# Performance work log

Measured on AMD Instinct MI355X. Metric: run time of the kernel, lower is better.

Reference implementation:

```python
import jax, jax.numpy as jnp
import numpy as np
import math

NUM_HEADS = 12
POS_BND = 16                 # patch_num
RPE_NUM = 2 * POS_BND + 1    # 33
LOGIT_SCALE_MAX = math.log(1.0 / 0.01)
EPS_NORM = 1e-12


def setup_inputs() -> dict:
    key = jax.random.key(0)
    ks = jax.random.split(key, 8)
    L, N, C = 257, 32, 768   # L = 16*16 patches + 1 CLS
    H, W = 16, 16
    x = jax.random.normal(ks[0], (L, N, C), dtype=jnp.float32)
    depth = jax.random.uniform(ks[1], (N, 1, H, W), dtype=jnp.float32)
    in_proj_w = jax.random.normal(ks[2], (3 * C, C), dtype=jnp.float32) * 0.02
    in_proj_b = jnp.zeros((3 * C,), dtype=jnp.float32)
    out_proj_w = jax.random.normal(ks[3], (C, C), dtype=jnp.float32) * 0.02
    out_proj_b = jnp.zeros((C,), dtype=jnp.float32)
    rpe_table = jax.random.normal(ks[4], (3 * RPE_NUM, NUM_HEADS), dtype=jnp.float32) * 0.02
    logit_scale = jnp.log(10.0) * jnp.ones((NUM_HEADS, 1, 1), dtype=jnp.float32)
    return {
        "x": x, "depth": depth,
        "in_proj_w": in_proj_w, "in_proj_b": in_proj_b,
        "out_proj_w": out_proj_w, "out_proj_b": out_proj_b,
        "rpe_table": rpe_table, "logit_scale": logit_scale,
    }


def _rpe_bias(depth, rpe_table):
    # depth: (B, 1, H, W) -> bias (B*num_heads, H*W, H*W)
    d = depth[:, 0]                              # (B, H, W)
    B, H, W = d.shape
    ii, jj = jnp.meshgrid(jnp.arange(H), jnp.arange(W), indexing="ij")
    xg = (jj.astype(jnp.float32) / (W - 1))[None].repeat(B, axis=0)   # (B,H,W)
    yg = (ii.astype(jnp.float32) / (H - 1))[None].repeat(B, axis=0)
    z_min = d.min(axis=(-2, -1), keepdims=True)
    z_max = d.max(axis=(-2, -1), keepdims=True)
    z = (d - z_min) / (z_max - z_min + 1e-8)
    coords = jnp.stack([xg, yg, z], axis=-1).reshape(B, H * W, 3)     # (B,HW,3)
    rel = coords[:, :, None, :] - coords[:, None, :, :]               # (B,HW,HW,3)
    idx = jnp.clip(jnp.round(rel * POS_BND).astype(jnp.int32), -POS_BND, POS_BND)
    idx = idx + POS_BND + jnp.arange(3, dtype=jnp.int32) * RPE_NUM    # (B,HW,HW,3)
    bias = rpe_table[idx].sum(axis=3)                                 # (B,HW,HW,heads)
    bias = bias.transpose(0, 3, 1, 2)                                 # (B,heads,HW,HW)
    return bias.reshape(-1, H * W, H * W)


def reference(x, depth, in_proj_w, in_proj_b, out_proj_w, out_proj_b, rpe_table, logit_scale):
    L, N, C = x.shape
    Hn = NUM_HEADS
    hd = C // Hn
    qkv = x @ in_proj_w.T + in_proj_b                     # (L,N,3C)
    q, k, v = jnp.split(qkv, 3, axis=-1)
    def to_heads(t):
        return t.reshape(L, N * Hn, hd).transpose(1, 0, 2)  # (N*Hn, L, hd)
    q, k, v = to_heads(q), to_heads(k), to_heads(v)
    # scaled-cosine attention: normalized q,k then clamped exp(log-scale)
    qn = q / jnp.maximum(jnp.linalg.norm(q, axis=-1, keepdims=True), EPS_NORM)
    kn = k / jnp.maximum(jnp.linalg.norm(k, axis=-1, keepdims=True), EPS_NORM)
    attn = jnp.einsum("bld,bmd->blm", qn, kn)             # (N*Hn, L, L)
    scale = jnp.exp(jnp.minimum(logit_scale, LOGIT_SCALE_MAX))   # (Hn,1,1)
    attn = (attn.reshape(N, Hn, L, L) * scale).reshape(N * Hn, L, L)
    # relative-position bias on patch tokens (skip CLS at index 0)
    res = _rpe_bias(depth, rpe_table)                     # (N*Hn, L-1, L-1)
    attn = attn.at[:, 1:, 1:].add(res)
    attn = jax.nn.softmax(attn, axis=-1)
    out = jnp.einsum("blm,bmd->bld", attn, v)             # (N*Hn, L, hd)
    out = out.transpose(1, 0, 2).reshape(L, N, C)
    out = out @ out_proj_w.T + out_proj_b
    return out, attn
```

## Files before the change

kernel.cpp:

```cpp
#include <hip/hip_runtime.h>
#include <math.h>

#define L_TOK 257
#define N_B 32
#define C_DIM 768
#define N_H 12
#define HD 64
#define BH (N_B * N_H)
#define M_TOK (L_TOK * N_B)
#define HW 256
#define RPE_NUM 33
#define LOGIT_MAX 4.6051701859880913680f
#define VT_STRIDE 264

typedef unsigned short ushort;
typedef unsigned int uint;
typedef __attribute__((ext_vector_type(8))) short short8;
typedef __attribute__((ext_vector_type(4))) float f32x4;

__device__ __forceinline__ ushort f2bf_rn(float f) {
  uint u = __float_as_uint(f);
  uint r = (u + 0x7FFF + ((u >> 16) & 1)) >> 16;
  return (ushort)r;
}
__device__ __forceinline__ float bf2f(ushort h) {
  return __uint_as_float(((uint)h) << 16);
}

__global__ __launch_bounds__(256)
void cvt_split(const float* __restrict__ src, ushort* __restrict__ hi,
               ushort* __restrict__ lo, int n) {
  int i = (blockIdx.x * 256 + threadIdx.x) * 4;
  if (i + 3 >= n + 3) return;
  if (i + 3 < n) {
    float4 v = *(const float4*)(src + i);
    ushort h0 = f2bf_rn(v.x), h1 = f2bf_rn(v.y), h2 = f2bf_rn(v.z), h3 = f2bf_rn(v.w);
    ushort l0 = f2bf_rn(v.x - bf2f(h0)), l1 = f2bf_rn(v.y - bf2f(h1));
    ushort l2 = f2bf_rn(v.z - bf2f(h2)), l3 = f2bf_rn(v.w - bf2f(h3));
    *(ushort4*)(hi + i) = make_ushort4(h0, h1, h2, h3);
    *(ushort4*)(lo + i) = make_ushort4(l0, l1, l2, l3);
  } else {
    for (int k = i; k < n; ++k) {
      float vv = src[k];
      ushort h = f2bf_rn(vv);
      hi[k] = h; lo[k] = f2bf_rn(vv - bf2f(h));
    }
  }
}

__global__ __launch_bounds__(256)
void gemm_mfma_split(const ushort* __restrict__ Ahi, const ushort* __restrict__ Alo,
                     const ushort* __restrict__ Bhi, const ushort* __restrict__ Blo,
                     const float* __restrict__ bias, float* __restrict__ Cout,
                     int M, int Nn, int K) {
  __shared__ __align__(16) ushort lds[4 * 128 * 32];
  ushort* sAh = lds;
  ushort* sAl = lds + 4096;
  ushort* sBh = lds + 8192;
  ushort* sBl = lds + 12288;

  const int t = threadIdx.x;
  const int wave = t >> 6, lane = t & 63;
  const int wm = (wave & 1) * 64;
  const int wn = (wave >> 1) * 64;
  const int m0 = blockIdx.x * 128;
  const int n0 = blockIdx.y * 128;

  const int ar = t >> 2;
  const int ac = (t & 3) * 8;
  const uint ldsOff = (uint)(t & 192) * 16;

  const int frm = lane & 15;
  const int frk = (lane >> 4) * 8;

  f32x4 acc[4][4] = {};

  for (int k0 = 0; k0 < K; k0 += 32) {
#pragma unroll
    for (int half = 0; half < 2; ++half) {
      int rA = m0 + half * 64 + ar; if (rA > M - 1) rA = M - 1;
      int rB = n0 + half * 64 + ar;
      size_t gA = (size_t)rA * K + k0 + ac;
      size_t gB = (size_t)rB * K + k0 + ac;
      uint so = (uint)half * 4096 + ldsOff;
      __builtin_amdgcn_global_load_lds(
          (const __attribute__((address_space(1))) void*)(Ahi + gA),
          (__attribute__((address_space(3))) void*)((char*)sAh + so), 16, 0, 0);
      __builtin_amdgcn_global_load_lds(
          (const __attribute__((address_space(1))) void*)(Alo + gA),
          (__attribute__((address_space(3))) void*)((char*)sAl + so), 16, 0, 0);
      __builtin_amdgcn_global_load_lds(
          (const __attribute__((address_space(1))) void*)(Bhi + gB),
          (__attribute__((address_space(3))) void*)((char*)sBh + so), 16, 0, 0);
      __builtin_amdgcn_global_load_lds(
          (const __attribute__((address_space(1))) void*)(Blo + gB),
          (__attribute__((address_space(3))) void*)((char*)sBl + so), 16, 0, 0);
    }
    __syncthreads();

    short8 ah[4], al[4], bh[4], bl[4];
#pragma unroll
    for (int i = 0; i < 4; ++i) {
      int r = wm + i * 16 + frm;
      ah[i] = *(const short8*)(sAh + r * 32 + frk);
      al[i] = *(const short8*)(sAl + r * 32 + frk);
      int c = wn + i * 16 + frm;
      bh[i] = *(const short8*)(sBh + c * 32 + frk);
      bl[i] = *(const short8*)(sBl + c * 32 + frk);
    }
#pragma unroll
    for (int i = 0; i < 4; ++i)
#pragma unroll
      for (int j = 0; j < 4; ++j) {
        acc[i][j] = __builtin_amdgcn_mfma_f32_16x16x32_bf16(ah[i], bh[j], acc[i][j], 0, 0, 0);
        acc[i][j] = __builtin_amdgcn_mfma_f32_16x16x32_bf16(ah[i], bl[j], acc[i][j], 0, 0, 0);
        acc[i][j] = __builtin_amdgcn_mfma_f32_16x16x32_bf16(al[i], bh[j], acc[i][j], 0, 0, 0);
      }
    __syncthreads();
  }

  const int ecol = lane & 15;
#pragma unroll
  for (int j = 0; j < 4; ++j) {
    int col = n0 + wn + j * 16 + ecol;
    float bv = bias[col];
#pragma unroll
    for (int i = 0; i < 4; ++i) {
      int rbase = m0 + wm + i * 16 + (lane >> 4) * 4;
#pragma unroll
      for (int r = 0; r < 4; ++r) {
        int row = rbase + r;
        if (row < M) Cout[(size_t)row * Nn + col] = acc[i][j][r] + bv;
      }
    }
  }
}

__global__ __launch_bounds__(256)
void repack_norm(const float* __restrict__ qkv,
                 ushort* __restrict__ qhi, ushort* __restrict__ qlo,
                 ushort* __restrict__ khi, ushort* __restrict__ klo,
                 float* __restrict__ v) {
  int gw = blockIdx.x * 4 + (threadIdx.x >> 6);
  int lane = threadIdx.x & 63;
  int b = gw / L_TOK, l = gw - b * L_TOK;
  int n = b / N_H, h = b - n * N_H;
  size_t base = (size_t)(l * N_B + n) * (3 * C_DIM) + h * HD + lane;
  float q = qkv[base];
  float k = qkv[base + C_DIM];
  float vv = qkv[base + 2 * C_DIM];
  float sq = q * q, sk = k * k;
#pragma unroll
  for (int o = 32; o > 0; o >>= 1) {
    sq += __shfl_down(sq, o);
    sk += __shfl_down(sk, o);
  }
  sq = __shfl(sq, 0);
  sk = __shfl(sk, 0);
  float iq = 1.0f / fmaxf(sqrtf(sq), 1e-12f);
  float ik = 1.0f / fmaxf(sqrtf(sk), 1e-12f);
  float qn_ = q * iq, kn_ = k * ik;
  size_t ob = (size_t)(b * L_TOK + l) * HD + lane;
  ushort qh = f2bf_rn(qn_);
  qhi[ob] = qh; qlo[ob] = f2bf_rn(qn_ - bf2f(qh));
  ushort kh = f2bf_rn(kn_);
  khi[ob] = kh; klo[ob] = f2bf_rn(kn_ - bf2f(kh));
  v[ob] = vv;
}

__global__ __launch_bounds__(256)
void vt_make(const float* __restrict__ v, ushort* __restrict__ vthi,
             ushort* __restrict__ vtlo) {
  __shared__ float sT[64][65];
  const int b = blockIdx.x;
  const int t = threadIdx.x;
  const float* vb = v + (size_t)b * L_TOK * HD;
  ushort* vh = vthi + (size_t)b * HD * VT_STRIDE;
  ushort* vl = vtlo + (size_t)b * HD * VT_STRIDE;
  for (int k0 = 0; k0 < 256; k0 += 64) {
#pragma unroll
    for (int p = 0; p < 16; ++p) {
      int idx = p * 256 + t;
      int k = idx >> 6, d = idx & 63;
      sT[d][k] = vb[(size_t)(k0 + k) * HD + d];
    }
    __syncthreads();
#pragma unroll
    for (int p = 0; p < 16; ++p) {
      int idx = p * 256 + t;
      int d = idx >> 6, k = idx & 63;
      float val = sT[d][k];
      ushort h = f2bf_rn(val);
      vh[(size_t)d * VT_STRIDE + k0 + k] = h;
      vl[(size_t)d * VT_STRIDE + k0 + k] = f2bf_rn(val - bf2f(h));
    }
    __syncthreads();
  }
  if (t < HD) {
    float val = vb[(size_t)256 * HD + t];
    ushort h = f2bf_rn(val);
    vh[(size_t)t * VT_STRIDE + 256] = h;
    vl[(size_t)t * VT_STRIDE + 256] = f2bf_rn(val - bf2f(h));
  }
}

__global__ __launch_bounds__(256)
void attn_mfma(const ushort* __restrict__ qhi, const ushort* __restrict__ qlo,
               const ushort* __restrict__ khi, const ushort* __restrict__ klo,
               const float* __restrict__ depth, const float* __restrict__ rpe,
               const float* __restrict__ lscale, float* __restrict__ P) {
  __shared__ __align__(16) ushort sKh[256 * 72];
  __shared__ __align__(16) ushort sKl[256 * 72];
  __shared__ float cz_s[HW];
  __shared__ float txd[32], tyd[32], tzt[36];
  __shared__ float red_s[16];
  __shared__ float s256[4][16];

  const int tile = blockIdx.x;
  const int b = blockIdx.y;
  const int n = b / N_H, h = b - n * N_H;
  const int t = threadIdx.x;
  const int lane = t & 63, wave = t >> 6;

  float dval = depth[n * HW + t];
  float mn = dval, mx = dval;
#pragma unroll
  for (int o = 32; o > 0; o >>= 1) {
    mn = fminf(mn, __shfl_down(mn, o));
    mx = fmaxf(mx, __shfl_down(mx, o));
  }
  if (lane == 0) { red_s[wave] = mn; red_s[8 + wave] = mx; }
  __syncthreads();
  float zmin = fminf(fminf(red_s[0], red_s[1]), fminf(red_s[2], red_s[3]));
  float zmax = fmaxf(fmaxf(red_s[8], red_s[9]), fmaxf(red_s[10], red_s[11]));
  float den = zmax - zmin + 1e-8f;
  cz_s[t] = (dval - zmin) / den;
  if (t < 31) {
    int d = t - 15;
    int ix = (int)rintf((float)d * (16.0f / 15.0f));
    ix = max(-16, min(16, ix));
    txd[t] = rpe[(ix + 16) * N_H + h];
    tyd[t] = rpe[(RPE_NUM + ix + 16) * N_H + h];
  }
  if (t < RPE_NUM) tzt[t] = rpe[(2 * RPE_NUM + t) * N_H + h];
  const float scale = expf(fminf(lscale[h], LOGIT_MAX));

  const ushort* khb = khi + (size_t)b * L_TOK * HD;
  const ushort* klb = klo + (size_t)b * L_TOK * HD;
#pragma unroll
  for (int it = 0; it < 8; ++it) {
    int idx = it * 256 + t;
    int j = idx >> 3, c = (idx & 7) * 8;
    *(uint4*)(sKh + j * 72 + c) = *(const uint4*)(khb + (size_t)j * HD + c);
    *(uint4*)(sKl + j * 72 + c) = *(const uint4*)(klb + (size_t)j * HD + c);
  }
  __syncthreads();

  const int qrow = tile * 64 + 16 * wave;
  const size_t qoff = ((size_t)b * L_TOK + qrow + (lane & 15)) * HD + (lane >> 4) * 8;
  short8 qh0 = *(const short8*)(qhi + qoff);
  short8 qh1 = *(const short8*)(qhi + qoff + 32);
  short8 ql0 = *(const short8*)(qlo + qoff);
  short8 ql1 = *(const short8*)(qlo + qoff + 32);

  f32x4 acc[16] = {};
#pragma unroll
  for (int jt = 0; jt < 16; ++jt) {
    const ushort* bp = sKh + (jt * 16 + (lane & 15)) * 72 + (lane >> 4) * 8;
    const ushort* bq = sKl + (jt * 16 + (lane & 15)) * 72 + (lane >> 4) * 8;
    short8 bh0 = *(const short8*)(bp);
    short8 bh1 = *(const short8*)(bp + 32);
    short8 bl0 = *(const short8*)(bq);
    short8 bl1 = *(const short8*)(bq + 32);
    acc[jt] = __builtin_amdgcn_mfma_f32_16x16x32_bf16(qh0, bh0, acc[jt], 0, 0, 0);
    acc[jt] = __builtin_amdgcn_mfma_f32_16x16x32_bf16(qh1, bh1, acc[jt], 0, 0, 0);
    acc[jt] = __builtin_amdgcn_mfma_f32_16x16x32_bf16(qh0, bl0, acc[jt], 0, 0, 0);
    acc[jt] = __builtin_amdgcn_mfma_f32_16x16x32_bf16(qh1, bl1, acc[jt], 0, 0, 0);
    acc[jt] = __builtin_amdgcn_mfma_f32_16x16x32_bf16(ql0, bh0, acc[jt], 0, 0, 0);
    acc[jt] = __builtin_amdgcn_mfma_f32_16x16x32_bf16(ql1, bh1, acc[jt], 0, 0, 0);
  }

  {
    const ushort* k6h = khb + (size_t)256 * HD + (lane >> 4) * 8;
    const ushort* k6l = klb + (size_t)256 * HD + (lane >> 4) * 8;
    float p = 0.f;
#pragma unroll
    for (int j = 0; j < 8; ++j) {
      float kf0 = bf2f(k6h[j]) + bf2f(k6l[j]);
      float kf1 = bf2f(k6h[32 + j]) + bf2f(k6l[32 + j]);
      float qf0 = bf2f((ushort)qh0[j]) + bf2f((ushort)ql0[j]);
      float qf1 = bf2f((ushort)qh1[j]) + bf2f((ushort)ql1[j]);
      p = fmaf(qf0, kf0, fmaf(qf1, kf1, p));
    }
    p += __shfl_xor(p, 16);
    p += __shfl_xor(p, 32);
    if (lane < 16) s256[wave][lane] = p;
  }

  const int g = lane >> 4, c0 = lane & 15;

  float lg6[4];
#pragma unroll
  for (int r = 0; r < 4; ++r) {
    int gi = tile * 64 + 16 * wave + 4 * g + r;
    float d6 = s256[wave][4 * g + r];
    float bz = 0.f;
    if (gi >= 1) {
      int dx = ((gi - 1) & 15) - 15;
      int dy = ((gi - 1) >> 4) - 15;
      float rz = (cz_s[gi - 1] - cz_s[255]) * 16.0f;
      int iz = (int)rintf(rz); iz = max(-16, min(16, iz));
      bz = txd[dx + 15] + tyd[dy + 15] + tzt[iz + 16];
    }
    lg6[r] = scale * d6 + bz;
  }

#pragma unroll
  for (int jt = 0; jt < 16; ++jt) {
    int col = jt * 16 + c0;
#pragma unroll
    for (int r = 0; r < 4; ++r) {
      int gi = tile * 64 + 16 * wave + 4 * g + r;
      float lv = scale * acc[jt][r];
      if (col >= 1 && gi >= 1) {
        int dx = ((gi - 1) & 15) - ((col - 1) & 15);
        int dy = ((gi - 1) >> 4) - ((col - 1) >> 4);
        float rz = (cz_s[gi - 1] - cz_s[col - 1]) * 16.0f;
        int iz = (int)rintf(rz); iz = max(-16, min(16, iz));
        lv += txd[dx + 15] + tyd[dy + 15] + tzt[iz + 16];
      }
      acc[jt][r] = lv;
    }
  }

  float* Pb_ = P + (size_t)b * L_TOK * L_TOK;
#pragma unroll
  for (int r = 0; r < 4; ++r) {
    int gi = tile * 64 + 16 * wave + 4 * g + r;
    float m = acc[0][r];
#pragma unroll
    for (int jt = 1; jt < 16; ++jt) m = fmaxf(m, acc[jt][r]);
#pragma unroll
    for (int o = 1; o < 16; o <<= 1) m = fmaxf(m, __shfl_xor(m, o));
    m = fmaxf(m, lg6[r]);
    float s = 0.f;
#pragma unroll
    for (int jt = 0; jt < 16; ++jt) {
      float e = __expf(acc[jt][r] - m);
      acc[jt][r] = e;
      s += e;
    }
#pragma unroll
    for (int o = 1; o < 16; o <<= 1) s += __shfl_xor(s, o);
    float e6 = __expf(lg6[r] - m);
    float inv = 1.0f / (s + e6);
    float* Prow = Pb_ + (size_t)gi * L_TOK;
#pragma unroll
    for (int jt = 0; jt < 16; ++jt)
      Prow[jt * 16 + c0] = acc[jt][r] * inv;
    if (c0 == 0) Prow[256] = e6 * inv;
  }
}

__global__ __launch_bounds__(256)
void attn_row256(const ushort* __restrict__ qhi, const ushort* __restrict__ qlo,
                 const ushort* __restrict__ khi, const ushort* __restrict__ klo,
                 const float* __restrict__ depth, const float* __restrict__ rpe,
                 const float* __restrict__ lscale, float* __restrict__ P) {
  __shared__ float qs[HD];
  __shared__ float cz_s[HW];
  __shared__ float txd[32], tyd[32], tzt[36];
  __shared__ float red_s[16];
  __shared__ float lg6_sh;

  const int b = blockIdx.x;
  const int n = b / N_H, h = b - n * N_H;
  const int t = threadIdx.x;
  const int lane = t & 63, wave = t >> 6;

  float dval = depth[n * HW + t];
  float mn = dval, mx = dval;
#pragma unroll
  for (int o = 32; o > 0; o >>= 1) {
    mn = fminf(mn, __shfl_down(mn, o));
    mx = fmaxf(mx, __shfl_down(mx, o));
  }
  if (lane == 0) { red_s[wave] = mn; red_s[8 + wave] = mx; }
  __syncthreads();
  float zmin = fminf(fminf(red_s[0], red_s[1]), fminf(red_s[2], red_s[3]));
  float zmax = fmaxf(fmaxf(red_s[8], red_s[9]), fmaxf(red_s[10], red_s[11]));
  float den = zmax - zmin + 1e-8f;
  cz_s[t] = (dval - zmin) / den;
  if (t < 31) {
    int d = t - 15;
    int ix = (int)rintf((float)d * (16.0f / 15.0f));
    ix = max(-16, min(16, ix));
    txd[t] = rpe[(ix + 16) * N_H + h];
    tyd[t] = rpe[(RPE_NUM + ix + 16) * N_H + h];
  }
  if (t < RPE_NUM) tzt[t] = rpe[(2 * RPE_NUM + t) * N_H + h];
  const float scale = expf(fminf(lscale[h], LOGIT_MAX));

  const size_t q6 = ((size_t)b * L_TOK + 256) * HD;
  if (t < HD) qs[t] = bf2f(qhi[q6 + t]) + bf2f(qlo[q6 + t]);
  __syncthreads();

  const ushort* krh = khi + ((size_t)b * L_TOK + t) * HD;
  const ushort* krl = klo + ((size_t)b * L_TOK + t) * HD;
  float dot = 0.f;
#pragma unroll
  for (int c = 0; c < HD; c += 8) {
    ushort4 hv0 = *(const ushort4*)(krh + c);
    ushort4 hv1 = *(const ushort4*)(krh + c + 4);
    ushort4 lv0 = *(const ushort4*)(krl + c);
    ushort4 lv1 = *(const ushort4*)(krl + c + 4);
    dot = fmaf(bf2f(hv0.x) + bf2f(lv0.x), qs[c + 0], dot);
    dot = fmaf(bf2f(hv0.y) + bf2f(lv0.y), qs[c + 1], dot);
    dot = fmaf(bf2f(hv0.z) + bf2f(lv0.z), qs[c + 2], dot);
    dot = fmaf(bf2f(hv0.w) + bf2f(lv0.w), qs[c + 3], dot);
    dot = fmaf(bf2f(hv1.x) + bf2f(lv1.x), qs[c + 4], dot);
    dot = fmaf(bf2f(hv1.y) + bf2f(lv1.y), qs[c + 5], dot);
    dot = fmaf(bf2f(hv1.z) + bf2f(lv1.z), qs[c + 6], dot);
    dot = fmaf(bf2f(hv1.w) + bf2f(lv1.w), qs[c + 7], dot);
  }

  float lg;
  {
    float bsum = 0.f;
    if (t >= 1) {
      int dx = 15 - ((t - 1) & 15);
      int dy = 15 - ((t - 1) >> 4);
      float rz = (cz_s[255] - cz_s[t - 1]) * 16.0f;
      int iz = (int)rintf(rz); iz = max(-16, min(16, iz));
      bsum = txd[dx + 15] + tyd[dy + 15] + tzt[iz + 16];
    }
    lg = scale * dot + bsum;
  }

  if (wave == 0) {
    const ushort* k6h = khi + q6;
    const ushort* k6l = klo + q6;
    float pp = (bf2f(k6h[lane]) + bf2f(k6l[lane])) * qs[lane];
#pragma unroll
    for (int o = 32; o > 0; o >>= 1) pp += __shfl_down(pp, o);
    if (lane == 0) {
      float bz = txd[15] + tyd[15] + tzt[16];
      lg6_sh = scale * pp + bz;
    }
  }

  float m = lg;
#pragma unroll
  for (int o = 32; o > 0; o >>= 1) m = fmaxf(m, __shfl_down(m, o));
  if (lane == 0) red_s[wave] = m;
  __syncthreads();
  float M = fmaxf(fmaxf(red_s[0], red_s[1]), fmaxf(red_s[2], red_s[3]));
  M = fmaxf(M, lg6_sh);
  float e = __expf(lg - M);
  float s = e;
#pragma unroll
  for (int o = 32; o > 0; o >>= 1) s += __shfl_down(s, o);
  if (lane == 0) red_s[8 + wave] = s;
  __syncthreads();
  float e6 = __expf(lg6_sh - M);
  float S = (red_s[8] + red_s[9]) + (red_s[10] + red_s[11]) + e6;
  float inv = 1.0f / S;
  float* Prow = P + (size_t)b * L_TOK * L_TOK + (size_t)256 * L_TOK;
  Prow[t] = e * inv;
  if (t == 0) Prow[256] = e6 * inv;
}

__global__ __launch_bounds__(256)
void pv_mfma(const float* __restrict__ P, const ushort* __restrict__ vthi,
             const ushort* __restrict__ vtlo, const float* __restrict__ v,
             float* __restrict__ out_lnc) {
  const int b = blockIdx.y;
  const int n = b / N_H, h = b - n * N_H;
  const int t = threadIdx.x;
  const int lane = t & 63, wave = t >> 6;
  const int rbase = blockIdx.x * 128 + wave * 32;
  const float* Pb = P + (size_t)b * L_TOK * L_TOK;
  const ushort* vh = vthi + (size_t)b * HD * VT_STRIDE;
  const ushort* vl = vtlo + (size_t)b * HD * VT_STRIDE;

  const int fm = lane & 15, fk = (lane >> 4) * 8;
  f32x4 acc[2][4] = {};

  for (int k0 = 0; k0 < 256; k0 += 32) {
    short8 ah[2], al[2], bh[4], bl[4];
#pragma unroll
    for (int i = 0; i < 2; ++i) {
      const float* pr = Pb + (size_t)(rbase + i * 16 + fm) * L_TOK + k0 + fk;
#pragma unroll
      for (int j = 0; j < 8; ++j) {
        float pv_ = pr[j];
        ushort hh = f2bf_rn(pv_);
        ah[i][j] = (short)hh;
        al[i][j] = (short)f2bf_rn(pv_ - bf2f(hh));
      }
    }
#pragma unroll
    for (int j = 0; j < 4; ++j) {
      const ushort* bp = vh + (size_t)(j * 16 + fm) * VT_STRIDE + k0 + fk;
      const ushort* bq = vl + (size_t)(j * 16 + fm) * VT_STRIDE + k0 + fk;
      bh[j] = *(const short8*)bp;
      bl[j] = *(const short8*)bq;
    }
#pragma unroll
    for (int i = 0; i < 2; ++i)
#pragma unroll
      for (int j = 0; j < 4; ++j) {
        acc[i][j] = __builtin_amdgcn_mfma_f32_16x16x32_bf16(ah[i], bh[j], acc[i][j], 0, 0, 0);
        acc[i][j] = __builtin_amdgcn_mfma_f32_16x16x32_bf16(ah[i], bl[j], acc[i][j], 0, 0, 0);
        acc[i][j] = __builtin_amdgcn_mfma_f32_16x16x32_bf16(al[i], bh[j], acc[i][j], 0, 0, 0);
        acc[i][j] = __builtin_amdgcn_mfma_f32_16x16x32_bf16(al[i], bl[j], acc[i][j], 0, 0, 0);
      }
  }

  const int g = lane >> 4;
  float v6[4];
#pragma unroll
  for (int j = 0; j < 4; ++j)
    v6[j] = v[((size_t)b * L_TOK + 256) * HD + j * 16 + fm];
#pragma unroll
  for (int i = 0; i < 2; ++i)
#pragma unroll
    for (int r = 0; r < 4; ++r) {
      int row = rbase + i * 16 + g * 4 + r;
      float p6 = Pb[(size_t)row * L_TOK + 256];
#pragma unroll
      for (int j = 0; j < 4; ++j) acc[i][j][r] += p6 * v6[j];
    }

#pragma unroll
  for (int i = 0; i < 2; ++i)
#pragma unroll
    for (int r = 0; r < 4; ++r) {
      int row = rbase + i * 16 + g * 4 + r;
      size_t o = ((size_t)row * N_B + n) * C_DIM + h * HD;
#pragma unroll
      for (int j = 0; j < 4; ++j)
        out_lnc[o + j * 16 + fm] = acc[i][j][r];
    }

  if (blockIdx.x == 0 && t < HD) {
    const float* Prow = Pb + (size_t)256 * L_TOK;
    const float* vb = v + (size_t)b * L_TOK * HD;
    float sum = 0.f;
    for (int k = 0; k < L_TOK; ++k)
      sum = fmaf(Prow[k], vb[(size_t)k * HD + t], sum);
    out_lnc[((size_t)256 * N_B + n) * C_DIM + h * HD + t] = sum;
  }
}

extern "C" void kernel_launch(void* const* d_in, const int* in_sizes, int n_in,
                              void* d_out, int out_size, void* d_ws, size_t ws_size,
                              hipStream_t stream) {
  const float* x      = (const float*)d_in[0];
  const float* depth  = (const float*)d_in[1];
  const float* w_in   = (const float*)d_in[2];
  const float* b_in   = (const float*)d_in[3];
  const float* w_out  = (const float*)d_in[4];
  const float* b_out  = (const float*)d_in[5];
  const float* rpe    = (const float*)d_in[6];
  const float* lscale = (const float*)d_in[7];
  float* out = (float*)d_out;
  float* ws = (float*)d_ws;

  float* qkv      = ws;
  float* attn_lnc = ws;
  float* v        = ws + 18948096;
  ushort* qhi = (ushort*)(ws + 25264128);
  ushort* qlo = qhi + 6316032;
  ushort* khi = qlo + 6316032;
  ushort* klo = khi + 6316032;
  ushort* wihi = (ushort*)(ws + 37896192);
  ushort* wilo = wihi + 1769472;
  ushort* wohi = wilo + 1769472;
  ushort* wolo = wohi + 589824;
  ushort* xhi = qhi;
  ushort* xlo = qlo;
  ushort* ahi = (ushort*)(qkv + 6316032);
  ushort* alo = ahi + 6316032;
  ushort* vthi = (ushort*)(ws + 6316032);
  ushort* vtlo = vthi + 6488064;
  float* Pout = out + 6316032;

  cvt_split<<<6168, 256, 0, stream>>>(x, xhi, xlo, 6316032);
  cvt_split<<<1728, 256, 0, stream>>>(w_in, wihi, wilo, 1769472);
  cvt_split<<<576, 256, 0, stream>>>(w_out, wohi, wolo, 589824);

  gemm_mfma_split<<<dim3(65, 18), 256, 0, stream>>>(xhi, xlo, wihi, wilo, b_in, qkv,
                                                    M_TOK, 3 * C_DIM, C_DIM);
  repack_norm<<<24672, 256, 0, stream>>>(qkv, qhi, qlo, khi, klo, v);
  vt_make<<<BH, 256, 0, stream>>>(v, vthi, vtlo);
  attn_mfma<<<dim3(4, BH), 256, 0, stream>>>(qhi, qlo, khi, klo, depth, rpe, lscale, Pout);
  attn_row256<<<BH, 256, 0, stream>>>(qhi, qlo, khi, klo, depth, rpe, lscale, Pout);
  pv_mfma<<<dim3(2, BH), 256, 0, stream>>>(Pout, vthi, vtlo, v, attn_lnc);

  cvt_split<<<6168, 256, 0, stream>>>(attn_lnc, ahi, alo, 6316032);
  gemm_mfma_split<<<dim3(65, 6), 256, 0, stream>>>(ahi, alo, wohi, wolo, b_out, out,
                                                   M_TOK, C_DIM, C_DIM);
}
```

Measured before the change: 522.7 us.

## Fuse QKV GEMM epilogue with head repack/normalization and fuse PV output split

The QKV GEMM epilogue now does the per-head L2 normalization, the bf16 hi/lo split and the scatter into head-major q/k/v buffers. This removes the separate repack_norm pass and the fp32 qkv intermediate. The PV kernel writes the bf16 hi/lo split of its output directly, which drops the cvt_split pass before the output projection. Both GEMMs switch to 1D grids with an XCD-aware block swizzle for better L2 locality; the epilogue's scattered stores may be less coalesced.

```diff
diff --git a/kernel.cpp b/kernel.cpp
--- a/kernel.cpp
+++ b/kernel.cpp
@@ -12,6 +12,8 @@
 #define RPE_NUM 33
 #define LOGIT_MAX 4.6051701859880913680f
 #define VT_STRIDE 264
+#define MT_Q 65
+#define NT_Q 18
 
 typedef unsigned short ushort;
 typedef unsigned int uint;
@@ -25,6 +27,13 @@
 }
 __device__ __forceinline__ float bf2f(ushort h) {
   return __uint_as_float(((uint)h) << 16);
+}
+
+__device__ __forceinline__ int xcd_swz(int wid, int nwg) {
+  int q = nwg >> 3, r = nwg & 7;
+  int xcd = wid & 7, pos = wid >> 3;
+  int base = (xcd < r) ? xcd * (q + 1) : r * (q + 1) + (xcd - r) * q;
+  return base + pos;
 }
 
 __global__ __launch_bounds__(256)
@@ -63,8 +72,10 @@
   const int wave = t >> 6, lane = t & 63;
   const int wm = (wave & 1) * 64;
   const int wn = (wave >> 1) * 64;
-  const int m0 = blockIdx.x * 128;
-  const int n0 = blockIdx.y * 128;
+  const int mt = (M + 127) >> 7;
+  const int wid = xcd_swz(blockIdx.x, gridDim.x);
+  const int m0 = (wid % mt) * 128;
+  const int n0 = (wid / mt) * 128;
 
   const int ar = t >> 2;
   const int ac = (t & 3) * 8;
@@ -137,35 +148,126 @@
 }
 
 __global__ __launch_bounds__(256)
-void repack_norm(const float* __restrict__ qkv,
-                 ushort* __restrict__ qhi, ushort* __restrict__ qlo,
-                 ushort* __restrict__ khi, ushort* __restrict__ klo,
-                 float* __restrict__ v) {
-  int gw = blockIdx.x * 4 + (threadIdx.x >> 6);
-  int lane = threadIdx.x & 63;
-  int b = gw / L_TOK, l = gw - b * L_TOK;
-  int n = b / N_H, h = b - n * N_H;
-  size_t base = (size_t)(l * N_B + n) * (3 * C_DIM) + h * HD + lane;
-  float q = qkv[base];
-  float k = qkv[base + C_DIM];
-  float vv = qkv[base + 2 * C_DIM];
-  float sq = q * q, sk = k * k;
-#pragma unroll
-  for (int o = 32; o > 0; o >>= 1) {
-    sq += __shfl_down(sq, o);
-    sk += __shfl_down(sk, o);
-  }
-  sq = __shfl(sq, 0);
-  sk = __shfl(sk, 0);
-  float iq = 1.0f / fmaxf(sqrtf(sq), 1e-12f);
-  float ik = 1.0f / fmaxf(sqrtf(sk), 1e-12f);
-  float qn_ = q * iq, kn_ = k * ik;
-  size_t ob = (size_t)(b * L_TOK + l) * HD + lane;
-  ushort qh = f2bf_rn(qn_);
-  qhi[ob] = qh; qlo[ob] = f2bf_rn(qn_ - bf2f(qh));
-  ushort kh = f2bf_rn(kn_);
-  khi[ob] = kh; klo[ob] = f2bf_rn(kn_ - bf2f(kh));
-  v[ob] = vv;
+void gemm_qkv_fused(const ushort* __restrict__ Ahi, const ushort* __restrict__ Alo,
+                    const ushort* __restrict__ Bhi, const ushort* __restrict__ Blo,
+                    const float* __restrict__ bias,
+                    ushort* __restrict__ qhi, ushort* __restrict__ qlo,
+                    ushort* __restrict__ khi, ushort* __restrict__ klo,
+                    float* __restrict__ vout) {
+  __shared__ __align__(16) ushort lds[4 * 128 * 32];
+  ushort* sAh = lds;
+  ushort* sAl = lds + 4096;
+  ushort* sBh = lds + 8192;
+  ushort* sBl = lds + 12288;
+
+  const int K = C_DIM, M = M_TOK;
+  const int t = threadIdx.x;
+  const int wave = t >> 6, lane = t & 63;
+  const int wm = (wave & 1) * 64;
+  const int wn = (wave >> 1) * 64;
+  const int wid = xcd_swz(blockIdx.x, MT_Q * NT_Q);
+  const int m0 = (wid % MT_Q) * 128;
+  const int n0 = (wid / MT_Q) * 128;
+
+  const int ar = t >> 2;
+  const int ac = (t & 3) * 8;
+  const uint ldsOff = (uint)(t & 192) * 16;
+
+  const int frm = lane & 15;
+  const int frk = (lane >> 4) * 8;
+
+  f32x4 acc[4][4] = {};
+
+  for (int k0 = 0; k0 < K; k0 += 32) {
+#pragma unroll
+    for (int half = 0; half < 2; ++half) {
+      int rA = m0 + half * 64 + ar; if (rA > M - 1) rA = M - 1;
+      int rB = n0 + half * 64 + ar;
+      size_t gA = (size_t)rA * K + k0 + ac;
+      size_t gB = (size_t)rB * K + k0 + ac;
+      uint so = (uint)half * 4096 + ldsOff;
+      __builtin_amdgcn_global_load_lds(
+          (const __attribute__((address_space(1))) void*)(Ahi + gA),
+          (__attribute__((address_space(3))) void*)((char*)sAh + so), 16, 0, 0);
+      __builtin_amdgcn_global_load_lds(
+          (const __attribute__((address_space(1))) void*)(Alo + gA),
+          (__attribute__((address_space(3))) void*)((char*)sAl + so), 16, 0, 0);
+      __builtin_amdgcn_global_load_lds(
+          (const __attribute__((address_space(1))) void*)(Bhi + gB),
+          (__attribute__((address_space(3))) void*)((char*)sBh + so), 16, 0, 0);
+      __builtin_amdgcn_global_load_lds(
+          (const __attribute__((address_space(1))) void*)(Blo + gB),
+          (__attribute__((address_space(3))) void*)((char*)sBl + so), 16, 0, 0);
+    }
+    __syncthreads();
+
+    short8 ah[4], al[4], bh[4], bl[4];
+#pragma unroll
+    for (int i = 0; i < 4; ++i) {
+      int r = wm + i * 16 + frm;
+      ah[i] = *(const short8*)(sAh + r * 32 + frk);
+      al[i] = *(const short8*)(sAl + r * 32 + frk);
+      int c = wn + i * 16 + frm;
+      bh[i] = *(const short8*)(sBh + c * 32 + frk);
+      bl[i] = *(const short8*)(sBl + c * 32 + frk);
+    }
+#pragma unroll
+    for (int i = 0; i < 4; ++i)
+#pragma unroll
+      for (int j = 0; j < 4; ++j) {
+        acc[i][j] = __builtin_amdgcn_mfma_f32_16x16x32_bf16(ah[i], bh[j], acc[i][j], 0, 0, 0);
+        acc[i][j] = __builtin_amdgcn_mfma_f32_16x16x32_bf16(ah[i], bl[j], acc[i][j], 0, 0, 0);
+        acc[i][j] = __builtin_amdgcn_mfma_f32_16x16x32_bf16(al[i], bh[j], acc[i][j], 0, 0, 0);
+      }
+    __syncthreads();
+  }
+
+  const int c0 = lane & 15, g = lane >> 4;
+  const int colBase = n0 + wn;
+  const int sect = colBase / C_DIM;
+  const int hh = (colBase - sect * C_DIM) >> 6;
+  float bv[4];
+#pragma unroll
+  for (int j = 0; j < 4; ++j) bv[j] = bias[colBase + j * 16 + c0];
+
+#pragma unroll
+  for (int i = 0; i < 4; ++i) {
+#pragma unroll
+    for (int r = 0; r < 4; ++r) {
+      const int row = m0 + wm + i * 16 + g * 4 + r;
+      float lv[4];
+#pragma unroll
+      for (int j = 0; j < 4; ++j) lv[j] = acc[i][j][r] + bv[j];
+      if (sect == 2) {
+        if (row < M) {
+          int l = row >> 5, n = row & 31;
+          size_t ob = ((size_t)((n * N_H + hh) * L_TOK + l)) * HD;
+#pragma unroll
+          for (int j = 0; j < 4; ++j) vout[ob + j * 16 + c0] = lv[j];
+        }
+      } else {
+        float ss = lv[0] * lv[0] + lv[1] * lv[1] + lv[2] * lv[2] + lv[3] * lv[3];
+        ss += __shfl_xor(ss, 1);
+        ss += __shfl_xor(ss, 2);
+        ss += __shfl_xor(ss, 4);
+        ss += __shfl_xor(ss, 8);
+        float inv = 1.0f / fmaxf(sqrtf(ss), 1e-12f);
+        if (row < M) {
+          int l = row >> 5, n = row & 31;
+          size_t ob = ((size_t)((n * N_H + hh) * L_TOK + l)) * HD;
+          ushort* dh = sect ? khi : qhi;
+          ushort* dl = sect ? klo : qlo;
+#pragma unroll
+          for (int j = 0; j < 4; ++j) {
+            float val = lv[j] * inv;
+            ushort hv = f2bf_rn(val);
+            dh[ob + j * 16 + c0] = hv;
+            dl[ob + j * 16 + c0] = f2bf_rn(val - bf2f(hv));
+          }
+        }
+      }
+    }
+  }
 }
 
 __global__ __launch_bounds__(256)
@@ -473,7 +575,7 @@
 __global__ __launch_bounds__(256)
 void pv_mfma(const float* __restrict__ P, const ushort* __restrict__ vthi,
              const ushort* __restrict__ vtlo, const float* __restrict__ v,
-             float* __restrict__ out_lnc) {
+             ushort* __restrict__ ahi, ushort* __restrict__ alo) {
   const int b = blockIdx.y;
   const int n = b / N_H, h = b - n * N_H;
   const int t = threadIdx.x;
@@ -539,8 +641,12 @@
       int row = rbase + i * 16 + g * 4 + r;
       size_t o = ((size_t)row * N_B + n) * C_DIM + h * HD;
 #pragma unroll
-      for (int j = 0; j < 4; ++j)
-        out_lnc[o + j * 16 + fm] = acc[i][j][r];
+      for (int j = 0; j < 4; ++j) {
+        float val = acc[i][j][r];
+        ushort hv = f2bf_rn(val);
+        ahi[o + j * 16 + fm] = hv;
+        alo[o + j * 16 + fm] = f2bf_rn(val - bf2f(hv));
+      }
     }
 
   if (blockIdx.x == 0 && t < HD) {
@@ -549,7 +655,10 @@
     float sum = 0.f;
     for (int k = 0; k < L_TOK; ++k)
       sum = fmaf(Prow[k], vb[(size_t)k * HD + t], sum);
-    out_lnc[((size_t)256 * N_B + n) * C_DIM + h * HD + t] = sum;
+    size_t o = ((size_t)256 * N_B + n) * C_DIM + h * HD + t;
+    ushort hv = f2bf_rn(sum);
+    ahi[o] = hv;
+    alo[o] = f2bf_rn(sum - bf2f(hv));
   }
 }
 
@@ -567,38 +676,34 @@
   float* out = (float*)d_out;
   float* ws = (float*)d_ws;
 
-  float* qkv      = ws;
-  float* attn_lnc = ws;
-  float* v        = ws + 18948096;
-  ushort* qhi = (ushort*)(ws + 25264128);
-  ushort* qlo = qhi + 6316032;
-  ushort* khi = qlo + 6316032;
-  ushort* klo = khi + 6316032;
+  ushort* xhi  = (ushort*)ws;
+  ushort* xlo  = xhi + 6316032;
+  ushort* vthi = (ushort*)(ws + 6316032);
+  ushort* vtlo = vthi + 6488064;
+  float*  v    = ws + 18948096;
+  ushort* qhi  = (ushort*)(ws + 25264128);
+  ushort* qlo  = qhi + 6316032;
+  ushort* khi  = qlo + 6316032;
+  ushort* klo  = khi + 6316032;
   ushort* wihi = (ushort*)(ws + 37896192);
   ushort* wilo = wihi + 1769472;
   ushort* wohi = wilo + 1769472;
   ushort* wolo = wohi + 589824;
-  ushort* xhi = qhi;
-  ushort* xlo = qlo;
-  ushort* ahi = (ushort*)(qkv + 6316032);
-  ushort* alo = ahi + 6316032;
-  ushort* vthi = (ushort*)(ws + 6316032);
-  ushort* vtlo = vthi + 6488064;
+  ushort* ahi  = xhi;
+  ushort* alo  = xlo;
   float* Pout = out + 6316032;
 
   cvt_split<<<6168, 256, 0, stream>>>(x, xhi, xlo, 6316032);
   cvt_split<<<1728, 256, 0, stream>>>(w_in, wihi, wilo, 1769472);
   cvt_split<<<576, 256, 0, stream>>>(w_out, wohi, wolo, 589824);
 
-  gemm_mfma_split<<<dim3(65, 18), 256, 0, stream>>>(xhi, xlo, wihi, wilo, b_in, qkv,
-                                                    M_TOK, 3 * C_DIM, C_DIM);
-  repack_norm<<<24672, 256, 0, stream>>>(qkv, qhi, qlo, khi, klo, v);
+  gemm_qkv_fused<<<MT_Q * NT_Q, 256, 0, stream>>>(xhi, xlo, wihi, wilo, b_in,
+                                                  qhi, qlo, khi, klo, v);
   vt_make<<<BH, 256, 0, stream>>>(v, vthi, vtlo);
   attn_mfma<<<dim3(4, BH), 256, 0, stream>>>(qhi, qlo, khi, klo, depth, rpe, lscale, Pout);
   attn_row256<<<BH, 256, 0, stream>>>(qhi, qlo, khi, klo, depth, rpe, lscale, Pout);
-  pv_mfma<<<dim3(2, BH), 256, 0, stream>>>(Pout, vthi, vtlo, v, attn_lnc);
-
-  cvt_split<<<6168, 256, 0, stream>>>(attn_lnc, ahi, alo, 6316032);
-  gemm_mfma_split<<<dim3(65, 6), 256, 0, stream>>>(ahi, alo, wohi, wolo, b_out, out,
-                                                   M_TOK, C_DIM, C_DIM);
-}
+  pv_mfma<<<dim3(2, BH), 256, 0, stream>>>(Pout, vthi, vtlo, v, ahi, alo);
+
+  gemm_mfma_split<<<65 * 6, 256, 0, stream>>>(ahi, alo, wohi, wolo, b_out, out,
+                                              M_TOK, C_DIM, C_DIM);
+}
```

Result: faster. 502.0 us (-4.0%).
